# Kernel optimization log

Hardware: AMD Instinct MI355X
Metric: run time of the kernel (lower is better)

Reference implementation:

```python
import jax, jax.numpy as jnp
import numpy as np

R, A, K, N = 4096, 101, 32, 4000000
AEC_LOW, AEC_SPAN = 0.0, 1.0
ETA_NEON, ETA_CHILD, ETA_ADULT = 2.0, 1.5, 1.0
SINK_M = 0.5
FEMALE_SHARE = 0.5
THETA_DEV, PHI_REP, THETA_CYC = 1.0, 1.0, 5.0
RATE_ANN, KAPPA = 0.02, 1.0
WA, RA = 15, 65
INHERIT_CONC, INHERIT_FRAC, BIRTH_ENDOW = 1.0, 0.8, 1.0


def setup_inputs() -> dict:
    key = jax.random.key(0)
    ks = jax.random.split(key, 26)
    dt = 1.0 / 365.0
    pop_age = jax.random.uniform(ks[8], (R, A)) * 1e4
    aging_M = jnp.eye(A) * (1.0 - dt) + jnp.eye(A, A, k=1) * dt
    aging_M = aging_M.at[A - 1, A - 1].set(1.0)
    return {
        'aec_r': jax.random.uniform(ks[0], (R,)) * 2.0,
        'gdp_pc_r': jax.random.uniform(ks[1], (R,)) * 5e4 + 1e3,
        'gdp_pc_ema_R': jax.random.uniform(ks[2], (R,)) * 5e4 + 1e3,
        'gdp_pc_baseline_R': jax.random.uniform(ks[3], (R,)) * 5e4 + 1e3,
        'dev_index_R': jax.random.uniform(ks[4], (R,)),
        'sink_use': jax.random.uniform(ks[5], (R,)),
        'sink_cap': jax.random.uniform(ks[6], (R,)) + 0.5,
        'hazard_A_base': jax.random.uniform(ks[7], (A,)) * 0.1 + 0.001,
        'pop_age': pop_age,
        'population': pop_age.sum(axis=1),
        'aging_M': aging_M,
        'asfr_vector': jax.random.uniform(ks[9], (35,)) * 0.2,
        'distance': jax.random.uniform(ks[10], (R, R)) * 100.0 + 1.0,
        'consump_w_age': jax.random.uniform(ks[11], (A,)),
        'participation_w_age': jax.random.uniform(ks[12], (A,)),
        'consump_base_R': jax.random.uniform(ks[13], (R,)) * 1e4 + 1e3,
        'labor_base_R': jax.random.uniform(ks[14], (R,)) * 1e4 + 1e3,
        'greed': jax.random.uniform(ks[15], (N,)) + 0.01,
        'eATP': jax.random.uniform(ks[16], (N,)) * 100.0,
        'eADP': jax.random.uniform(ks[17], (N,)) * 100.0,
        'eAMP': jax.random.uniform(ks[18], (N,)) * 100.0,
        'pool_atp_R': jax.random.uniform(ks[19], (R,)) * 1e6,
        'pool_adp_R': jax.random.uniform(ks[20], (R,)) * 1e6,
        'pool_amp_R': jax.random.uniform(ks[21], (R,)) * 1e6,
        'nbr_idx': jax.random.randint(ks[22], (R, K), 0, R),
        'agent_region': jax.random.randint(ks[23], (N,), 0, R),
    }


def _forward(aec_r, gdp_pc_r, gdp_pc_ema_R, gdp_pc_baseline_R, dev_index_R, sink_use, sink_cap,
             hazard_A_base, pop_age, population, aging_M, asfr_vector, distance, consump_w_age,
             participation_w_age, consump_base_R, labor_base_R, greed, eATP, eADP, eAMP,
             pool_atp_R, pool_adp_R, pool_amp_R, nbr_idx, agent_region):
    eps = 1e-9
    dt = 1.0 / 365.0
    aec_norm = jnp.clip((aec_r - AEC_LOW) / AEC_SPAN, 0.0, 1.0)
    gdp_prev = gdp_pc_ema_R
    gdp_ema = gdp_prev * 0.9 + 0.1 * gdp_pc_r
    g_ratio = jnp.log(jnp.maximum(gdp_ema / (gdp_pc_baseline_R + eps), 1e-6))
    g_term = jnp.clip(0.5 + 0.5 * jnp.tanh(0.5 * g_ratio), 0.0, 1.0)
    util = jnp.clip(sink_use / (sink_cap + eps), 0.0, 1.0)
    H = jnp.clip(0.5 * aec_norm + 0.4 * g_term + 0.1 * (1.0 - util), 0.0, 1.0)
    dev_proxy = jnp.clip(0.5 + 0.5 * jnp.tanh(0.3 * g_ratio), 0.0, 1.0)
    dev = dev_index_R * 0.99 + 0.01 * dev_proxy
    # age-bucketed hazard multipliers: age 0 / ages 1..14 / ages 15+
    ages = jnp.arange(A)[None, :]
    m_neon = jnp.exp(-ETA_NEON * H)[:, None]
    m_child = jnp.exp(-ETA_CHILD * H)[:, None]
    m_adult = jnp.exp(-ETA_ADULT * H)[:, None]
    mult = jnp.where(ages == 0, m_neon, jnp.where(ages < 15, m_child, m_adult))
    haz = jnp.clip(hazard_A_base[None, :] * mult * (1.0 + SINK_M * util[:, None]), 0.0, 5.0)
    S = jnp.exp(-haz * dt)
    survivors = pop_age * S
    pop_after = survivors @ aging_M  # [R, A]
    deaths_R = jnp.maximum(pop_age.sum(1) - survivors.sum(1), 0.0)
    death_frac_R = jnp.clip(deaths_R / (population + eps), 0.0, 0.99)
    # fertility
    female_RF = FEMALE_SHARE * pop_after[:, 15:50]
    surv_u5 = jnp.exp(-haz[:, 0:5].sum(1))
    F_dev = jnp.clip(jnp.exp(-THETA_DEV * dev), 0.5, 1.5)
    F_rep = jnp.clip((0.995 / jnp.maximum(surv_u5, 1e-3)) ** PHI_REP, 0.5, 1.8)
    g_growth = jnp.log(jnp.maximum(gdp_ema + eps, 1e-6)) - jnp.log(jnp.maximum(gdp_prev + eps, 1e-6))
    F_cyc = jnp.clip(jnp.exp(-THETA_CYC * jnp.maximum(-g_growth, 0.0)), 0.6, 1.2)
    F_total = jnp.clip(F_dev * F_rep * F_cyc, 0.4, 1.8)
    births = jnp.maximum((female_RF * asfr_vector[None, :]).sum(1) * F_total * dt, 0.0)
    births_surv = births * jnp.exp(-haz[:, 0] * dt)
    pop_after = pop_after.at[:, 0].add(births_surv)
    # migration gather-scatter over neighbor regions
    a0, a1 = 18, 40
    mobile = pop_after[:, a0:a1]
    attract = 0.6 * (gdp_pc_r / (gdp_pc_baseline_R + eps)) + 0.4 * (0.5 + 0.5 * aec_norm)
    attract = attract / (attract.mean() + eps)
    dist = jnp.take_along_axis(distance, nbr_idx, axis=1)  # [R, K]
    cost = 1.0 + dist / (dist.mean() + eps)
    w = jax.nn.relu(attract[nbr_idx] / cost ** KAPPA)
    w = w / (w.sum(1, keepdims=True) + eps)
    frac_move = min(max(RATE_ANN * dt, 0.0), 0.25)
    out_R = mobile.sum(1) * frac_move
    move = out_R[:, None] * w  # [R, K]
    age_share = mobile / (mobile.sum(1, keepdims=True) + eps)
    pop_after = pop_after.at[:, a0:a1].add(-age_share * move.sum(1, keepdims=True))
    inflow = (age_share[:, None, :] * move[:, :, None]).reshape(R * K, a1 - a0)
    add = jnp.zeros((R, a1 - a0), pop_after.dtype).at[nbr_idx.reshape(-1)].add(inflow)
    pop_after = pop_after.at[:, a0:a1].add(add)
    pop_new = jnp.maximum(pop_after, 0.0)
    population_new = jnp.maximum(pop_new.sum(1), 0.0)
    consump_scale = jnp.clip((pop_new * consump_w_age[None, :]).sum(1) / (consump_base_R + eps), 0.25, 4.0)
    labor_factor = jnp.clip((pop_new * participation_w_age[None, :]).sum(1) / (labor_base_R + eps), 0.2, 1.2)
    work = pop_new[:, WA:RA].sum(1)
    young = pop_new[:, :WA].sum(1)
    old = pop_new[:, RA:].sum(1)
    psr = work / (old + eps)
    dep = (young + old) / (work + eps)
    # agent-level death / inheritance scatters
    dfi = death_frac_R[agent_region]
    w_raw = (greed + 1e-9) ** INHERIT_CONC
    w_sum_r = jax.ops.segment_sum(w_raw, agent_region, num_segments=R)
    w_norm = w_raw / (w_sum_r[agent_region] + eps)

    def settle(wallet, pool):
        removed = wallet * dfi
        removed_pool = jax.ops.segment_sum(removed, agent_region, num_segments=R)
        heir_pool = removed_pool * INHERIT_FRAC
        wallet2 = wallet - removed + w_norm * heir_pool[agent_region]
        return wallet2, pool - (removed_pool - heir_pool)

    eATP2, pool_atp2 = settle(eATP, pool_atp_R)
    eADP2, pool_adp2 = settle(eADP, pool_adp_R)
    eAMP2, pool_amp2 = settle(eAMP, pool_amp_R)
    counts = jax.ops.segment_sum(jnp.ones_like(dfi), agent_region, num_segments=R)
    eATP2 = eATP2 + BIRTH_ENDOW * (births_surv / jnp.maximum(counts, 1.0))[agent_region]
    return (pop_new, population_new, gdp_ema, dev, H, consump_scale, labor_factor, psr, dep,
            eATP2, eADP2, eAMP2, pool_atp2, pool_adp2, pool_amp2)


def reference(aec_r, gdp_pc_r, gdp_pc_ema_R, gdp_pc_baseline_R, dev_index_R, sink_use, sink_cap,
              hazard_A_base, pop_age, population, aging_M, asfr_vector, distance, consump_w_age,
              participation_w_age, consump_base_R, labor_base_R, greed, eATP, eADP, eAMP,
              pool_atp_R, pool_adp_R, pool_amp_R, nbr_idx, agent_region):
    return _forward(aec_r, gdp_pc_r, gdp_pc_ema_R, gdp_pc_baseline_R, dev_index_R, sink_use,
                    sink_cap, hazard_A_base, pop_age, population, aging_M, asfr_vector, distance,
                    consump_w_age, participation_w_age, consump_base_R, labor_base_R, greed,
                    eATP, eADP, eAMP, pool_atp_R, pool_adp_R, pool_amp_R, nbr_idx, agent_region)
```

## Files before the change

kernel.cpp:

```cpp
#include <hip/hip_runtime.h>

#define RR 4096
#define AA 101
#define PAD_W 104
#define KK 32
#define NAG 4000000

#define NCHUNK 32
#define DR 512
#define NRANGE 8
#define EPB (RR * KK / NCHUNK)
#define NB 512
#define NMIG (NRANGE * NCHUNK)
#define CH 16

static constexpr float EPS  = 1e-9f;
static constexpr float DT   = 1.0f / 365.0f;
static constexpr float FRAC_MOVE = 0.02f / 365.0f;

static constexpr float SC2   = 4.0f;
static constexpr float INV2  = 0.25f;
static constexpr float SC9   = 512.0f;
static constexpr float INV9  = 1.0f / 512.0f;
static constexpr float SC18  = 262144.0f;
static constexpr float INV18 = 1.0f / 262144.0f;

#define OUT_POP   0
#define OUT_POPN  413696
#define OUT_GDP   417792
#define OUT_DEV   421888
#define OUT_H     425984
#define OUT_CONS  430080
#define OUT_LAB   434176
#define OUT_PSR   438272
#define OUT_DEP   442368
#define OUT_ATP   446464
#define OUT_ADP   4446464
#define OUT_AMP   8446464
#define OUT_PATP  12446464
#define OUT_PADP  12450560
#define OUT_PAMP  12454656

static __device__ __forceinline__ float clampf(float x, float lo, float hi) {
    return fminf(fmaxf(x, lo), hi);
}
static __device__ __forceinline__ float wred(float x) {
#pragma unroll
    for (int m = 32; m; m >>= 1) x += __shfl_xor(x, m);
    return x;
}

__global__ __launch_bounds__(256) void k_region1(
    const float* __restrict__ aec, const float* __restrict__ gdp_pc,
    const float* __restrict__ gdp_ema_in, const float* __restrict__ gdp_base,
    const float* __restrict__ dev_in, const float* __restrict__ sink_use,
    const float* __restrict__ sink_cap, const float* __restrict__ haz_base,
    const float* __restrict__ pop_age, const float* __restrict__ population,
    const float* __restrict__ aging, const float* __restrict__ asfr,
    const float* __restrict__ distance, const int* __restrict__ nbr,
    float* __restrict__ Wpa, float* __restrict__ Wdfrac, float* __restrict__ Wbsurv,
    float* __restrict__ Wattr, float* __restrict__ Wgdist, float* __restrict__ Wdsum,
    float* __restrict__ O)
{
    int wid = threadIdx.x >> 6, lane = threadIdx.x & 63;
    int r = blockIdx.x * 4 + wid;

    float aec_norm = clampf(aec[r], 0.0f, 1.0f);
    float gprev = gdp_ema_in[r];
    float gema  = gprev * 0.9f + 0.1f * gdp_pc[r];
    float base  = gdp_base[r];
    float g_ratio = logf(fmaxf(gema / (base + EPS), 1e-6f));
    float g_term  = clampf(0.5f + 0.5f * tanhf(0.5f * g_ratio), 0.0f, 1.0f);
    float util = clampf(sink_use[r] / (sink_cap[r] + EPS), 0.0f, 1.0f);
    float H = clampf(0.5f * aec_norm + 0.4f * g_term + 0.1f * (1.0f - util), 0.0f, 1.0f);
    float dev_proxy = clampf(0.5f + 0.5f * tanhf(0.3f * g_ratio), 0.0f, 1.0f);
    float dev = dev_in[r] * 0.99f + 0.01f * dev_proxy;

    float m_neon  = expf(-2.0f * H);
    float m_child = expf(-1.5f * H);
    float m_adult = expf(-1.0f * H);
    float hazmul = 1.0f + 0.5f * util;

    int a0 = lane * 2, a1 = a0 + 1;
    bool v0 = (a0 < AA), v1 = (a1 < AA);

    float p0 = 0.f, p1 = 0.f, hz0 = 0.f, hz1 = 0.f;
    if (v0) {
        p0 = pop_age[r * AA + a0];
        float mult = (a0 == 0) ? m_neon : ((a0 < 15) ? m_child : m_adult);
        hz0 = clampf(haz_base[a0] * mult * hazmul, 0.0f, 5.0f);
    }
    if (v1) {
        p1 = pop_age[r * AA + a1];
        float mult = (a1 < 15) ? m_child : m_adult;
        hz1 = clampf(haz_base[a1] * mult * hazmul, 0.0f, 5.0f);
    }
    float s0 = v0 ? p0 * expf(-hz0 * DT) : 0.f;
    float s1 = v1 ? p1 * expf(-hz1 * DT) : 0.f;
    float sp = __shfl_up(s1, 1);

    float Md0 = 0.f, Md1 = 0.f, Ms0 = 0.f, Ms1 = 0.f;
    if (v0) { Md0 = aging[a0 * AA + a0]; if (a0 > 0) Ms0 = aging[(a0 - 1) * AA + a0]; }
    if (v1) { Md1 = aging[a1 * AA + a1]; Ms1 = aging[(a1 - 1) * AA + a1]; }

    float pa0 = v0 ? ((a0 == 0) ? s0 * Md0 : s0 * Md0 + sp * Ms0) : 0.f;
    float pa1 = v1 ? (s1 * Md1 + s0 * Ms1) : 0.f;

    if (v0 && a0 > 0) Wpa[r * PAD_W + a0] = pa0;
    if (v1)           Wpa[r * PAD_W + a1] = pa1;

    float pop_sum  = wred(p0 + p1);
    float surv_sum = wred(s0 + s1);
    float haz05 = wred(((v0 && a0 < 5) ? hz0 : 0.f) + ((v1 && a1 < 5) ? hz1 : 0.f));
    float bs0 = (a0 >= 15 && a0 < 50) ? 0.5f * pa0 * asfr[a0 - 15] : 0.f;
    float bs1 = (a1 >= 15 && a1 < 50) ? 0.5f * pa1 * asfr[a1 - 15] : 0.f;
    float b_sum = wred(bs0 + bs1);

    float dc = 0.f;
    if (lane < KK) {
        int idx = nbr[r * KK + lane];
        float d = distance[(size_t)r * RR + idx];
        Wgdist[r * KK + lane] = d;
        dc = d;
    }
    float dsum = wred(dc);

    if (lane == 0) {
        O[OUT_GDP + r] = gema;
        O[OUT_DEV + r] = dev;
        O[OUT_H + r]   = H;

        float deaths = fmaxf(pop_sum - surv_sum, 0.0f);
        Wdfrac[r] = clampf(deaths / (population[r] + EPS), 0.0f, 0.99f);

        float surv_u5 = expf(-haz05);
        float F_dev = clampf(expf(-dev), 0.5f, 1.5f);
        float F_rep = clampf(0.995f / fmaxf(surv_u5, 0.001f), 0.5f, 1.8f);
        float g_growth = logf(fmaxf(gema + EPS, 1e-6f)) - logf(fmaxf(gprev + EPS, 1e-6f));
        float F_cyc = clampf(expf(-5.0f * fmaxf(-g_growth, 0.0f)), 0.6f, 1.2f);
        float F_total = clampf(F_dev * F_rep * F_cyc, 0.4f, 1.8f);
        float births = fmaxf(b_sum * F_total * DT, 0.0f);
        float bsurv = births * expf(-hz0 * DT);
        Wbsurv[r] = bsurv;
        Wpa[r * PAD_W + 0] = pa0 + bsurv;

        Wattr[r] = 0.6f * (gdp_pc[r] / (base + EPS)) + 0.4f * (0.5f + 0.5f * aec_norm);
        Wdsum[r] = dsum;
    }
}

__global__ __launch_bounds__(256) void k_migrate_a(
    const int* __restrict__ nbr, const float* __restrict__ Wattr,
    const float* __restrict__ Wgdist, const float* __restrict__ Wdsum,
    float* __restrict__ Wpa, float* __restrict__ Wash, float* __restrict__ Wmove)
{
    __shared__ float sred[8];
    int t = threadIdx.x;
    {
        float a = 0.f, d = 0.f;
        for (int i = t; i < RR; i += 256) { a += Wattr[i]; d += Wdsum[i]; }
        a = wred(a); d = wred(d);
        int w0 = t >> 6;
        if ((t & 63) == 0) { sred[w0] = a; sred[4 + w0] = d; }
    }
    __syncthreads();
    float asum = sred[0] + sred[1] + sred[2] + sred[3];
    float dall = sred[4] + sred[5] + sred[6] + sred[7];
    float inv_am = 1.0f / (asum / (float)RR + EPS);
    float inv_dm = 1.0f / (dall / (float)(RR * KK) + EPS);

    int wid = t >> 6, lane = t & 63;
    int r = blockIdx.x * 4 + wid;

    float mob = 0.f;
    if (lane < 22) mob = Wpa[r * PAD_W + 18 + lane];
    float msum = wred(lane < 22 ? mob : 0.f);

    float w = 0.f;
    if (lane < KK) {
        int idx = nbr[r * KK + lane];
        float an = Wattr[idx] * inv_am;
        float cost = 1.0f + Wgdist[r * KK + lane] * inv_dm;
        w = fmaxf(an / cost, 0.0f);
    }
    float wsum = wred(lane < KK ? w : 0.f);

    float out_R = msum * FRAC_MOVE;
    float invw = 1.0f / (wsum + EPS);
    float move_sum = out_R * wsum * invw;
    float inv_ms = 1.0f / (msum + EPS);

    if (lane < 22) {
        float ash = mob * inv_ms;
        Wash[r * 22 + lane] = ash;
        Wpa[r * PAD_W + 18 + lane] = mob - ash * move_sum;
    }
    if (lane < KK) Wmove[r * KK + lane] = out_R * w * invw;
}

__global__ __launch_bounds__(512) void k_migbhist(
    const int* __restrict__ nbr, const float* __restrict__ Wash,
    const float* __restrict__ Wmove, float* __restrict__ Smig,
    const int* __restrict__ reg, const float* __restrict__ greed,
    const float* __restrict__ atp, const float* __restrict__ adp,
    const float* __restrict__ amp, unsigned long long* __restrict__ S)
{
    __shared__ unsigned long long h[11 * DR];
    int bid = blockIdx.x;

    if (bid < NMIG) {
        int range = bid & (NRANGE - 1);
        int chunk = bid >> 3;
        int d0 = range * DR;

        for (int i = threadIdx.x; i < 11 * DR; i += 512) h[i] = 0ull;
        __syncthreads();

        int tend = (chunk + 1) * EPB;
        for (int t = chunk * EPB + threadIdx.x; t < tend; t += 512) {
            int idx = nbr[t];
            if (idx >= d0 && idx < d0 + DR) {
                int rsrc = t >> 5;
                float mv = Wmove[t];
                const float* ash = &Wash[rsrc * 22];
                int dl = idx - d0;
#pragma unroll
                for (int f = 0; f < 11; f++) {
                    unsigned long long lo = __float2uint_rn(ash[2 * f] * mv * SC18);
                    unsigned long long hi = __float2uint_rn(ash[2 * f + 1] * mv * SC18);
                    atomicAdd(&h[f * DR + dl], lo | (hi << 32));
                }
            }
        }
        __syncthreads();

        for (int i = threadIdx.x; i < 11 * DR; i += 512) {
            int f = i / DR, d = i - f * DR;
            unsigned long long v = h[i];
            Smig[(chunk * 22 + 2 * f) * RR + d0 + d]     = (float)(unsigned int)v * INV18;
            Smig[(chunk * 22 + 2 * f + 1) * RR + d0 + d] = (float)(v >> 32) * INV18;
        }
    } else {
        int b = bid - NMIG;
        for (int i = threadIdx.x; i < RR; i += 512) h[i] = 0ull;
        __syncthreads();

        const int4*   reg4 = (const int4*)reg;
        const float4* g4 = (const float4*)greed;
        const float4* a4 = (const float4*)atp;
        const float4* d4 = (const float4*)adp;
        const float4* m4 = (const float4*)amp;
        const int NQ = NAG / 4;
        const int STRIDE = NB * 512;

        for (int q = b * 512 + threadIdx.x; q < NQ; q += STRIDE) {
            int4 rr = reg4[q];
            float4 gv = g4[q], av = a4[q], dv = d4[q], mv = m4[q];
#define DO1(RX, GX, AX, DX, MX) { \
            unsigned long long ai = __float2uint_rn((AX) * SC2); \
            unsigned long long di = __float2uint_rn((DX) * SC2); \
            unsigned long long mi = __float2uint_rn((MX) * SC2); \
            unsigned long long gi = __float2uint_rn(((GX) + 1e-9f) * SC9); \
            atomicAdd(&h[RX], ai | (di << 14) | (mi << 28) | (gi << 42) | (1ull << 56)); }
            DO1(rr.x, gv.x, av.x, dv.x, mv.x)
            DO1(rr.y, gv.y, av.y, dv.y, mv.y)
            DO1(rr.z, gv.z, av.z, dv.z, mv.z)
            DO1(rr.w, gv.w, av.w, dv.w, mv.w)
#undef DO1
        }
        __syncthreads();

        for (int i = threadIdx.x; i < RR; i += 512)
            S[(size_t)b * RR + i] = h[i];
    }
}

__global__ __launch_bounds__(256) void k_reduce(
    const unsigned long long* __restrict__ S, const float* __restrict__ Smig,
    float* __restrict__ T, float* __restrict__ Wadd)
{
    int blk = blockIdx.x;
    if (blk < 256) {
        int tid = blk * 256 + threadIdx.x;
        int r = tid & (RR - 1);
        int c = tid >> 12;
        const int bpc = NB / CH;
        float sa = 0.f, sd = 0.f, sm = 0.f, sg = 0.f, sc = 0.f;
        for (int b = c * bpc; b < (c + 1) * bpc; b++) {
            unsigned long long p = S[(size_t)b * RR + r];
            sa += (float)(unsigned int)(p & 0x3FFFull);
            sd += (float)(unsigned int)((p >> 14) & 0x3FFFull);
            sm += (float)(unsigned int)((p >> 28) & 0x3FFFull);
            sg += (float)(unsigned int)((p >> 42) & 0x3FFFull);
            sc += (float)(unsigned int)(p >> 56);
        }
        T[(0 * CH + c) * RR + r] = sa * INV2;
        T[(1 * CH + c) * RR + r] = sd * INV2;
        T[(2 * CH + c) * RR + r] = sm * INV2;
        T[(3 * CH + c) * RR + r] = sg * INV9;
        T[(4 * CH + c) * RR + r] = sc;
    } else {
        int t2 = (blk - 256) * 256 + threadIdx.x;
        int f = t2 >> 12, rr = t2 & (RR - 1);
        float acc = 0.f;
#pragma unroll
        for (int c = 0; c < NCHUNK; c++)
            acc += Smig[(c * 22 + f) * RR + rr];
        Wadd[rr * 24 + f] = acc;
    }
}

__global__ __launch_bounds__(256) void k_fin(
    const float* __restrict__ Wpa, const float* __restrict__ Wadd,
    const float* __restrict__ cw, const float* __restrict__ pw,
    const float* __restrict__ cbase, const float* __restrict__ lbase,
    const float* __restrict__ T,
    const float* __restrict__ Wdfrac, const float* __restrict__ Wbsurv,
    const float* __restrict__ patp, const float* __restrict__ padp,
    const float* __restrict__ pamp,
    float4* __restrict__ P4, float2* __restrict__ P2,
    float* __restrict__ O)
{
    int blk = blockIdx.x;
    if (blk < 1024) {
        int wid = threadIdx.x >> 6, lane = threadIdx.x & 63;
        int r = blk * 4 + wid;
        int a0 = lane * 2, a1 = a0 + 1;
        bool v0 = (a0 < AA), v1 = (a1 < AA);

        float va = 0.f, vb = 0.f;
        if (lane < 51) {
            float2 pp = *(const float2*)&Wpa[r * PAD_W + a0];
            va = pp.x; vb = pp.y;
        }
        if (a0 >= 18 && a0 < 40) {
            float2 ad = *(const float2*)&Wadd[r * 24 + (a0 - 18)];
            va += ad.x; vb += ad.y;
        }
        va = v0 ? fmaxf(va, 0.0f) : 0.f;
        vb = v1 ? fmaxf(vb, 0.0f) : 0.f;
        if (v0) O[OUT_POP + r * AA + a0] = va;
        if (v1) O[OUT_POP + r * AA + a1] = vb;

        float cw0 = v0 ? cw[a0] : 0.f, cw1 = v1 ? cw[a1] : 0.f;
        float pw0 = v0 ? pw[a0] : 0.f, pw1 = v1 ? pw[a1] : 0.f;

        float psum  = wred(va + vb);
        float cdot  = wred(va * cw0 + vb * cw1);
        float ldot  = wred(va * pw0 + vb * pw1);
        float young = wred(((a0 < 15) ? va : 0.f) + ((a1 < 15) ? vb : 0.f));
        float work  = wred(((a0 >= 15 && a0 < 65) ? va : 0.f) + ((a1 >= 15 && a1 < 65) ? vb : 0.f));
        float old   = wred(((a0 >= 65) ? va : 0.f) + ((a1 >= 65) ? vb : 0.f));

        if (lane == 0) {
            O[OUT_POPN + r] = fmaxf(psum, 0.0f);
            O[OUT_CONS + r] = clampf(cdot / (cbase[r] + EPS), 0.25f, 4.0f);
            O[OUT_LAB + r]  = clampf(ldot / (lbase[r] + EPS), 0.2f, 1.2f);
            O[OUT_PSR + r]  = work / (old + EPS);
            O[OUT_DEP + r]  = (young + old) / (work + EPS);
        }
    } else {
        int r = (blk - 1024) * 256 + threadIdx.x;
        if (r >= RR) return;
        float sums[5];
#pragma unroll
        for (int s = 0; s < 5; s++) {
            float acc = 0.f;
#pragma unroll
            for (int c = 0; c < CH; c++)
                acc += T[(s * CH + c) * RR + r];
            sums[s] = acc;
        }
        float dfi = Wdfrac[r];
        float ra = sums[0] * dfi;
        float rd = sums[1] * dfi;
        float rm = sums[2] * dfi;
        O[OUT_PATP + r] = patp[r] - ra * 0.2f;
        O[OUT_PADP + r] = padp[r] - rd * 0.2f;
        O[OUT_PAMP + r] = pamp[r] - rm * 0.2f;
        P4[r] = make_float4(1.0f - dfi, 1.0f / (sums[3] + EPS), ra * 0.8f, rd * 0.8f);
        P2[r] = make_float2(rm * 0.8f, Wbsurv[r] / fmaxf(sums[4], 1.0f));
    }
}

__global__ __launch_bounds__(256) void k_apply(
    const int* __restrict__ reg, const float* __restrict__ greed,
    const float* __restrict__ atp, const float* __restrict__ adp,
    const float* __restrict__ amp,
    const float4* __restrict__ P4, const float2* __restrict__ P2,
    float* __restrict__ O)
{
    int q = blockIdx.x * 256 + threadIdx.x;
    if (q >= NAG / 4) return;
    int4 rr = ((const int4*)reg)[q];
    float4 g = ((const float4*)greed)[q];
    float4 a = ((const float4*)atp)[q];
    float4 d = ((const float4*)adp)[q];
    float4 m = ((const float4*)amp)[q];
    float4 oa, od, om;
#define ONE(c) { float4 t4 = P4[rr.c]; float2 t2 = P2[rr.c]; \
    float wn = (g.c + 1e-9f) * t4.y; \
    oa.c = a.c * t4.x + wn * t4.z + t2.y; \
    od.c = d.c * t4.x + wn * t4.w; \
    om.c = m.c * t4.x + wn * t2.x; }
    ONE(x) ONE(y) ONE(z) ONE(w)
#undef ONE
    ((float4*)(O + OUT_ATP))[q] = oa;
    ((float4*)(O + OUT_ADP))[q] = od;
    ((float4*)(O + OUT_AMP))[q] = om;
}

extern "C" void kernel_launch(void* const* d_in, const int* in_sizes, int n_in,
                              void* d_out, int out_size, void* d_ws, size_t ws_size,
                              hipStream_t stream) {
    const float* aec       = (const float*)d_in[0];
    const float* gdp_pc    = (const float*)d_in[1];
    const float* gdp_ema   = (const float*)d_in[2];
    const float* gdp_base  = (const float*)d_in[3];
    const float* dev_in    = (const float*)d_in[4];
    const float* sink_use  = (const float*)d_in[5];
    const float* sink_cap  = (const float*)d_in[6];
    const float* haz_base  = (const float*)d_in[7];
    const float* pop_age   = (const float*)d_in[8];
    const float* population= (const float*)d_in[9];
    const float* aging     = (const float*)d_in[10];
    const float* asfr      = (const float*)d_in[11];
    const float* distance  = (const float*)d_in[12];
    const float* cw        = (const float*)d_in[13];
    const float* pw        = (const float*)d_in[14];
    const float* cbase     = (const float*)d_in[15];
    const float* lbase     = (const float*)d_in[16];
    const float* greed     = (const float*)d_in[17];
    const float* eATP      = (const float*)d_in[18];
    const float* eADP      = (const float*)d_in[19];
    const float* eAMP      = (const float*)d_in[20];
    const float* patp      = (const float*)d_in[21];
    const float* padp      = (const float*)d_in[22];
    const float* pamp      = (const float*)d_in[23];
    const int*   nbr       = (const int*)d_in[24];
    const int*   reg       = (const int*)d_in[25];

    float* O = (float*)d_out;

    float* W = (float*)d_ws;
    float* Wpa    = W;
    float* Wdfrac = Wpa    + RR * PAD_W;
    float* Wbsurv = Wdfrac + RR;
    float* Wattr  = Wbsurv + RR;
    float* Wdsum  = Wattr  + RR;
    float* Wgdist = Wdsum  + RR;
    float* Wash   = Wgdist + RR * KK;
    float* Wmove  = Wash   + RR * 22;
    float* P4f    = Wmove  + RR * KK;
    float* P2f    = P4f    + RR * 4;
    float* Wadd   = P2f    + RR * 2;
    float* T      = Wadd   + RR * 24;
    float* Smig   = T      + 5 * CH * RR;
    unsigned long long* S = (unsigned long long*)(Smig + (size_t)NCHUNK * 22 * RR);

    k_region1<<<RR / 4, 256, 0, stream>>>(
        aec, gdp_pc, gdp_ema, gdp_base, dev_in, sink_use, sink_cap, haz_base,
        pop_age, population, aging, asfr, distance, nbr,
        Wpa, Wdfrac, Wbsurv, Wattr, Wgdist, Wdsum, O);

    k_migrate_a<<<RR / 4, 256, 0, stream>>>(nbr, Wattr, Wgdist, Wdsum, Wpa, Wash, Wmove);

    k_migbhist<<<NMIG + NB, 512, 0, stream>>>(
        nbr, Wash, Wmove, Smig, reg, greed, eATP, eADP, eAMP, S);

    k_reduce<<<256 + (22 * RR) / 256, 256, 0, stream>>>(S, Smig, T, Wadd);

    k_fin<<<1024 + RR / 256, 256, 0, stream>>>(
        Wpa, Wadd, cw, pw, cbase, lbase, T, Wdfrac, Wbsurv,
        patp, padp, pamp, (float4*)P4f, (float2*)P2f, O);

    k_apply<<<(NAG / 4 + 255) / 256, 256, 0, stream>>>(
        reg, greed, eATP, eADP, eAMP, (const float4*)P4f, (const float2*)P2f, O);
}
```

Measured before the change: 97.12 us.

## Move agent histogram into region kernel and regroup reduce stages

The per-agent packed-atomic histogram moves out of the migration kernel and into the first region kernel as extra blocks. It now runs alongside the per-region demography and no longer waits for the migration-weight stage. The histogram loop now prefetches the next strided iteration's loads before doing the current iteration's atomics. The S-to-T reduction moves into the migration-scatter kernel's trailing blocks, and the Smig fold becomes its own kernel, so the launch count stays the same. The first kernel's shared memory grows to 32KB for all blocks, which may lower occupancy for the region blocks.

```diff
diff --git a/kernel.cpp b/kernel.cpp
--- a/kernel.cpp
+++ b/kernel.cpp
@@ -50,7 +50,7 @@
     return x;
 }
 
-__global__ __launch_bounds__(256) void k_region1(
+__global__ __launch_bounds__(256) void k_r1hist(
     const float* __restrict__ aec, const float* __restrict__ gdp_pc,
     const float* __restrict__ gdp_ema_in, const float* __restrict__ gdp_base,
     const float* __restrict__ dev_in, const float* __restrict__ sink_use,
@@ -60,92 +60,143 @@
     const float* __restrict__ distance, const int* __restrict__ nbr,
     float* __restrict__ Wpa, float* __restrict__ Wdfrac, float* __restrict__ Wbsurv,
     float* __restrict__ Wattr, float* __restrict__ Wgdist, float* __restrict__ Wdsum,
+    const int* __restrict__ reg, const float* __restrict__ greed,
+    const float* __restrict__ atp, const float* __restrict__ adp,
+    const float* __restrict__ amp, unsigned long long* __restrict__ S,
     float* __restrict__ O)
 {
-    int wid = threadIdx.x >> 6, lane = threadIdx.x & 63;
-    int r = blockIdx.x * 4 + wid;
-
-    float aec_norm = clampf(aec[r], 0.0f, 1.0f);
-    float gprev = gdp_ema_in[r];
-    float gema  = gprev * 0.9f + 0.1f * gdp_pc[r];
-    float base  = gdp_base[r];
-    float g_ratio = logf(fmaxf(gema / (base + EPS), 1e-6f));
-    float g_term  = clampf(0.5f + 0.5f * tanhf(0.5f * g_ratio), 0.0f, 1.0f);
-    float util = clampf(sink_use[r] / (sink_cap[r] + EPS), 0.0f, 1.0f);
-    float H = clampf(0.5f * aec_norm + 0.4f * g_term + 0.1f * (1.0f - util), 0.0f, 1.0f);
-    float dev_proxy = clampf(0.5f + 0.5f * tanhf(0.3f * g_ratio), 0.0f, 1.0f);
-    float dev = dev_in[r] * 0.99f + 0.01f * dev_proxy;
-
-    float m_neon  = expf(-2.0f * H);
-    float m_child = expf(-1.5f * H);
-    float m_adult = expf(-1.0f * H);
-    float hazmul = 1.0f + 0.5f * util;
-
-    int a0 = lane * 2, a1 = a0 + 1;
-    bool v0 = (a0 < AA), v1 = (a1 < AA);
-
-    float p0 = 0.f, p1 = 0.f, hz0 = 0.f, hz1 = 0.f;
-    if (v0) {
-        p0 = pop_age[r * AA + a0];
-        float mult = (a0 == 0) ? m_neon : ((a0 < 15) ? m_child : m_adult);
-        hz0 = clampf(haz_base[a0] * mult * hazmul, 0.0f, 5.0f);
-    }
-    if (v1) {
-        p1 = pop_age[r * AA + a1];
-        float mult = (a1 < 15) ? m_child : m_adult;
-        hz1 = clampf(haz_base[a1] * mult * hazmul, 0.0f, 5.0f);
-    }
-    float s0 = v0 ? p0 * expf(-hz0 * DT) : 0.f;
-    float s1 = v1 ? p1 * expf(-hz1 * DT) : 0.f;
-    float sp = __shfl_up(s1, 1);
-
-    float Md0 = 0.f, Md1 = 0.f, Ms0 = 0.f, Ms1 = 0.f;
-    if (v0) { Md0 = aging[a0 * AA + a0]; if (a0 > 0) Ms0 = aging[(a0 - 1) * AA + a0]; }
-    if (v1) { Md1 = aging[a1 * AA + a1]; Ms1 = aging[(a1 - 1) * AA + a1]; }
-
-    float pa0 = v0 ? ((a0 == 0) ? s0 * Md0 : s0 * Md0 + sp * Ms0) : 0.f;
-    float pa1 = v1 ? (s1 * Md1 + s0 * Ms1) : 0.f;
-
-    if (v0 && a0 > 0) Wpa[r * PAD_W + a0] = pa0;
-    if (v1)           Wpa[r * PAD_W + a1] = pa1;
-
-    float pop_sum  = wred(p0 + p1);
-    float surv_sum = wred(s0 + s1);
-    float haz05 = wred(((v0 && a0 < 5) ? hz0 : 0.f) + ((v1 && a1 < 5) ? hz1 : 0.f));
-    float bs0 = (a0 >= 15 && a0 < 50) ? 0.5f * pa0 * asfr[a0 - 15] : 0.f;
-    float bs1 = (a1 >= 15 && a1 < 50) ? 0.5f * pa1 * asfr[a1 - 15] : 0.f;
-    float b_sum = wred(bs0 + bs1);
-
-    float dc = 0.f;
-    if (lane < KK) {
-        int idx = nbr[r * KK + lane];
-        float d = distance[(size_t)r * RR + idx];
-        Wgdist[r * KK + lane] = d;
-        dc = d;
-    }
-    float dsum = wred(dc);
-
-    if (lane == 0) {
-        O[OUT_GDP + r] = gema;
-        O[OUT_DEV + r] = dev;
-        O[OUT_H + r]   = H;
-
-        float deaths = fmaxf(pop_sum - surv_sum, 0.0f);
-        Wdfrac[r] = clampf(deaths / (population[r] + EPS), 0.0f, 0.99f);
-
-        float surv_u5 = expf(-haz05);
-        float F_dev = clampf(expf(-dev), 0.5f, 1.5f);
-        float F_rep = clampf(0.995f / fmaxf(surv_u5, 0.001f), 0.5f, 1.8f);
-        float g_growth = logf(fmaxf(gema + EPS, 1e-6f)) - logf(fmaxf(gprev + EPS, 1e-6f));
-        float F_cyc = clampf(expf(-5.0f * fmaxf(-g_growth, 0.0f)), 0.6f, 1.2f);
-        float F_total = clampf(F_dev * F_rep * F_cyc, 0.4f, 1.8f);
-        float births = fmaxf(b_sum * F_total * DT, 0.0f);
-        float bsurv = births * expf(-hz0 * DT);
-        Wbsurv[r] = bsurv;
-        Wpa[r * PAD_W + 0] = pa0 + bsurv;
-
-        Wattr[r] = 0.6f * (gdp_pc[r] / (base + EPS)) + 0.4f * (0.5f + 0.5f * aec_norm);
-        Wdsum[r] = dsum;
+    __shared__ unsigned long long h[RR];
+    int blk = blockIdx.x;
+
+    if (blk < 1024) {
+        int wid = threadIdx.x >> 6, lane = threadIdx.x & 63;
+        int r = blk * 4 + wid;
+
+        float aec_norm = clampf(aec[r], 0.0f, 1.0f);
+        float gprev = gdp_ema_in[r];
+        float gema  = gprev * 0.9f + 0.1f * gdp_pc[r];
+        float base  = gdp_base[r];
+        float g_ratio = logf(fmaxf(gema / (base + EPS), 1e-6f));
+        float g_term  = clampf(0.5f + 0.5f * tanhf(0.5f * g_ratio), 0.0f, 1.0f);
+        float util = clampf(sink_use[r] / (sink_cap[r] + EPS), 0.0f, 1.0f);
+        float H = clampf(0.5f * aec_norm + 0.4f * g_term + 0.1f * (1.0f - util), 0.0f, 1.0f);
+        float dev_proxy = clampf(0.5f + 0.5f * tanhf(0.3f * g_ratio), 0.0f, 1.0f);
+        float dev = dev_in[r] * 0.99f + 0.01f * dev_proxy;
+
+        float m_neon  = expf(-2.0f * H);
+        float m_child = expf(-1.5f * H);
+        float m_adult = expf(-1.0f * H);
+        float hazmul = 1.0f + 0.5f * util;
+
+        int a0 = lane * 2, a1 = a0 + 1;
+        bool v0 = (a0 < AA), v1 = (a1 < AA);
+
+        float p0 = 0.f, p1 = 0.f, hz0 = 0.f, hz1 = 0.f;
+        if (v0) {
+            p0 = pop_age[r * AA + a0];
+            float mult = (a0 == 0) ? m_neon : ((a0 < 15) ? m_child : m_adult);
+            hz0 = clampf(haz_base[a0] * mult * hazmul, 0.0f, 5.0f);
+        }
+        if (v1) {
+            p1 = pop_age[r * AA + a1];
+            float mult = (a1 < 15) ? m_child : m_adult;
+            hz1 = clampf(haz_base[a1] * mult * hazmul, 0.0f, 5.0f);
+        }
+        float s0 = v0 ? p0 * expf(-hz0 * DT) : 0.f;
+        float s1 = v1 ? p1 * expf(-hz1 * DT) : 0.f;
+        float sp = __shfl_up(s1, 1);
+
+        float Md0 = 0.f, Md1 = 0.f, Ms0 = 0.f, Ms1 = 0.f;
+        if (v0) { Md0 = aging[a0 * AA + a0]; if (a0 > 0) Ms0 = aging[(a0 - 1) * AA + a0]; }
+        if (v1) { Md1 = aging[a1 * AA + a1]; Ms1 = aging[(a1 - 1) * AA + a1]; }
+
+        float pa0 = v0 ? ((a0 == 0) ? s0 * Md0 : s0 * Md0 + sp * Ms0) : 0.f;
+        float pa1 = v1 ? (s1 * Md1 + s0 * Ms1) : 0.f;
+
+        if (v0 && a0 > 0) Wpa[r * PAD_W + a0] = pa0;
+        if (v1)           Wpa[r * PAD_W + a1] = pa1;
+
+        float pop_sum  = wred(p0 + p1);
+        float surv_sum = wred(s0 + s1);
+        float haz05 = wred(((v0 && a0 < 5) ? hz0 : 0.f) + ((v1 && a1 < 5) ? hz1 : 0.f));
+        float bs0 = (a0 >= 15 && a0 < 50) ? 0.5f * pa0 * asfr[a0 - 15] : 0.f;
+        float bs1 = (a1 >= 15 && a1 < 50) ? 0.5f * pa1 * asfr[a1 - 15] : 0.f;
+        float b_sum = wred(bs0 + bs1);
+
+        float dc = 0.f;
+        if (lane < KK) {
+            int idx = nbr[r * KK + lane];
+            float d = distance[(size_t)r * RR + idx];
+            Wgdist[r * KK + lane] = d;
+            dc = d;
+        }
+        float dsum = wred(dc);
+
+        if (lane == 0) {
+            O[OUT_GDP + r] = gema;
+            O[OUT_DEV + r] = dev;
+            O[OUT_H + r]   = H;
+
+            float deaths = fmaxf(pop_sum - surv_sum, 0.0f);
+            Wdfrac[r] = clampf(deaths / (population[r] + EPS), 0.0f, 0.99f);
+
+            float surv_u5 = expf(-haz05);
+            float F_dev = clampf(expf(-dev), 0.5f, 1.5f);
+            float F_rep = clampf(0.995f / fmaxf(surv_u5, 0.001f), 0.5f, 1.8f);
+            float g_growth = logf(fmaxf(gema + EPS, 1e-6f)) - logf(fmaxf(gprev + EPS, 1e-6f));
+            float F_cyc = clampf(expf(-5.0f * fmaxf(-g_growth, 0.0f)), 0.6f, 1.2f);
+            float F_total = clampf(F_dev * F_rep * F_cyc, 0.4f, 1.8f);
+            float births = fmaxf(b_sum * F_total * DT, 0.0f);
+            float bsurv = births * expf(-hz0 * DT);
+            Wbsurv[r] = bsurv;
+            Wpa[r * PAD_W + 0] = pa0 + bsurv;
+
+            Wattr[r] = 0.6f * (gdp_pc[r] / (base + EPS)) + 0.4f * (0.5f + 0.5f * aec_norm);
+            Wdsum[r] = dsum;
+        }
+    } else {
+        int b = blk - 1024;
+        for (int i = threadIdx.x; i < RR; i += 256) h[i] = 0ull;
+        __syncthreads();
+
+        const int4*   reg4 = (const int4*)reg;
+        const float4* g4 = (const float4*)greed;
+        const float4* a4 = (const float4*)atp;
+        const float4* d4 = (const float4*)adp;
+        const float4* m4 = (const float4*)amp;
+        const int NQ = NAG / 4;
+        const int STRIDE = NB * 256;
+
+        int q = b * 256 + threadIdx.x;
+        if (q < NQ) {
+            int4 rA = reg4[q];
+            float4 gA = g4[q], aA = a4[q], dA = d4[q], mA = m4[q];
+            while (true) {
+                int qn = q + STRIDE;
+                bool more = (qn < NQ);
+                int qs = more ? qn : q;
+                int4 rB = reg4[qs];
+                float4 gB = g4[qs], aB = a4[qs], dB = d4[qs], mB = m4[qs];
+#define DO1(RX, GX, AX, DX, MX) { \
+                unsigned long long ai = __float2uint_rn((AX) * SC2); \
+                unsigned long long di = __float2uint_rn((DX) * SC2); \
+                unsigned long long mi = __float2uint_rn((MX) * SC2); \
+                unsigned long long gi = __float2uint_rn(((GX) + 1e-9f) * SC9); \
+                atomicAdd(&h[RX], ai | (di << 14) | (mi << 28) | (gi << 42) | (1ull << 56)); }
+                DO1(rA.x, gA.x, aA.x, dA.x, mA.x)
+                DO1(rA.y, gA.y, aA.y, dA.y, mA.y)
+                DO1(rA.z, gA.z, aA.z, dA.z, mA.z)
+                DO1(rA.w, gA.w, aA.w, dA.w, mA.w)
+#undef DO1
+                if (!more) break;
+                rA = rB; gA = gB; aA = aB; dA = dB; mA = mB;
+                q = qn;
+            }
+        }
+        __syncthreads();
+
+        for (int i = threadIdx.x; i < RR; i += 256)
+            S[(size_t)b * RR + i] = h[i];
     }
 }
 
@@ -198,12 +249,10 @@
     if (lane < KK) Wmove[r * KK + lane] = out_R * w * invw;
 }
 
-__global__ __launch_bounds__(512) void k_migbhist(
+__global__ __launch_bounds__(512) void k_mbdec(
     const int* __restrict__ nbr, const float* __restrict__ Wash,
     const float* __restrict__ Wmove, float* __restrict__ Smig,
-    const int* __restrict__ reg, const float* __restrict__ greed,
-    const float* __restrict__ atp, const float* __restrict__ adp,
-    const float* __restrict__ amp, unsigned long long* __restrict__ S)
+    const unsigned long long* __restrict__ S, float* __restrict__ T)
 {
     __shared__ unsigned long long h[11 * DR];
     int bid = blockIdx.x;
@@ -241,47 +290,7 @@
             Smig[(chunk * 22 + 2 * f + 1) * RR + d0 + d] = (float)(v >> 32) * INV18;
         }
     } else {
-        int b = bid - NMIG;
-        for (int i = threadIdx.x; i < RR; i += 512) h[i] = 0ull;
-        __syncthreads();
-
-        const int4*   reg4 = (const int4*)reg;
-        const float4* g4 = (const float4*)greed;
-        const float4* a4 = (const float4*)atp;
-        const float4* d4 = (const float4*)adp;
-        const float4* m4 = (const float4*)amp;
-        const int NQ = NAG / 4;
-        const int STRIDE = NB * 512;
-
-        for (int q = b * 512 + threadIdx.x; q < NQ; q += STRIDE) {
-            int4 rr = reg4[q];
-            float4 gv = g4[q], av = a4[q], dv = d4[q], mv = m4[q];
-#define DO1(RX, GX, AX, DX, MX) { \
-            unsigned long long ai = __float2uint_rn((AX) * SC2); \
-            unsigned long long di = __float2uint_rn((DX) * SC2); \
-            unsigned long long mi = __float2uint_rn((MX) * SC2); \
-            unsigned long long gi = __float2uint_rn(((GX) + 1e-9f) * SC9); \
-            atomicAdd(&h[RX], ai | (di << 14) | (mi << 28) | (gi << 42) | (1ull << 56)); }
-            DO1(rr.x, gv.x, av.x, dv.x, mv.x)
-            DO1(rr.y, gv.y, av.y, dv.y, mv.y)
-            DO1(rr.z, gv.z, av.z, dv.z, mv.z)
-            DO1(rr.w, gv.w, av.w, dv.w, mv.w)
-#undef DO1
-        }
-        __syncthreads();
-
-        for (int i = threadIdx.x; i < RR; i += 512)
-            S[(size_t)b * RR + i] = h[i];
-    }
-}
-
-__global__ __launch_bounds__(256) void k_reduce(
-    const unsigned long long* __restrict__ S, const float* __restrict__ Smig,
-    float* __restrict__ T, float* __restrict__ Wadd)
-{
-    int blk = blockIdx.x;
-    if (blk < 256) {
-        int tid = blk * 256 + threadIdx.x;
+        int tid = (bid - NMIG) * 512 + threadIdx.x;
         int r = tid & (RR - 1);
         int c = tid >> 12;
         const int bpc = NB / CH;
@@ -299,15 +308,19 @@
         T[(2 * CH + c) * RR + r] = sm * INV2;
         T[(3 * CH + c) * RR + r] = sg * INV9;
         T[(4 * CH + c) * RR + r] = sc;
-    } else {
-        int t2 = (blk - 256) * 256 + threadIdx.x;
-        int f = t2 >> 12, rr = t2 & (RR - 1);
-        float acc = 0.f;
+    }
+}
+
+__global__ __launch_bounds__(256) void k_fold(
+    const float* __restrict__ Smig, float* __restrict__ Wadd)
+{
+    int t2 = blockIdx.x * 256 + threadIdx.x;
+    int f = t2 >> 12, rr = t2 & (RR - 1);
+    float acc = 0.f;
 #pragma unroll
-        for (int c = 0; c < NCHUNK; c++)
-            acc += Smig[(c * 22 + f) * RR + rr];
-        Wadd[rr * 24 + f] = acc;
-    }
+    for (int c = 0; c < NCHUNK; c++)
+        acc += Smig[(c * 22 + f) * RR + rr];
+    Wadd[rr * 24 + f] = acc;
 }
 
 __global__ __launch_bounds__(256) void k_fin(
@@ -458,17 +471,17 @@
     float* Smig   = T      + 5 * CH * RR;
     unsigned long long* S = (unsigned long long*)(Smig + (size_t)NCHUNK * 22 * RR);
 
-    k_region1<<<RR / 4, 256, 0, stream>>>(
+    k_r1hist<<<1024 + NB, 256, 0, stream>>>(
         aec, gdp_pc, gdp_ema, gdp_base, dev_in, sink_use, sink_cap, haz_base,
         pop_age, population, aging, asfr, distance, nbr,
-        Wpa, Wdfrac, Wbsurv, Wattr, Wgdist, Wdsum, O);
+        Wpa, Wdfrac, Wbsurv, Wattr, Wgdist, Wdsum,
+        reg, greed, eATP, eADP, eAMP, S, O);
 
     k_migrate_a<<<RR / 4, 256, 0, stream>>>(nbr, Wattr, Wgdist, Wdsum, Wpa, Wash, Wmove);
 
-    k_migbhist<<<NMIG + NB, 512, 0, stream>>>(
-        nbr, Wash, Wmove, Smig, reg, greed, eATP, eADP, eAMP, S);
-
-    k_reduce<<<256 + (22 * RR) / 256, 256, 0, stream>>>(S, Smig, T, Wadd);
+    k_mbdec<<<NMIG + 128, 512, 0, stream>>>(nbr, Wash, Wmove, Smig, S, T);
+
+    k_fold<<<(22 * RR) / 256, 256, 0, stream>>>(Smig, Wadd);
 
     k_fin<<<1024 + RR / 256, 256, 0, stream>>>(
         Wpa, Wadd, cw, pw, cbase, lbase, T, Wdfrac, Wbsurv,
```

New measurement: 92.81 us. 1.05x faster.

## Move agent histogram into region kernel and decode S alongside migration

Applied to the files above, without the earlier changes.

The per-agent packed shared-memory histogram moves out of the migration kernel into the first region kernel. Both now run as 1024-thread blocks in one launch, so the 4M-agent streaming pass overlaps with the per-region demographics instead of running after migrate_a. The S decode (per-chunk summation into T) moves into the migration kernel's extra blocks, and the Smig fold becomes its own small kernel. The launch count stays the same, but block sizes and the dependency order change, and the 1024-thread blocks may lower occupancy.

```diff
diff --git a/kernel.cpp b/kernel.cpp
--- a/kernel.cpp
+++ b/kernel.cpp
@@ -50,7 +50,7 @@
     return x;
 }
 
-__global__ __launch_bounds__(256) void k_region1(
+__global__ __launch_bounds__(1024) void k_r1hist(
     const float* __restrict__ aec, const float* __restrict__ gdp_pc,
     const float* __restrict__ gdp_ema_in, const float* __restrict__ gdp_base,
     const float* __restrict__ dev_in, const float* __restrict__ sink_use,
@@ -60,92 +60,132 @@
     const float* __restrict__ distance, const int* __restrict__ nbr,
     float* __restrict__ Wpa, float* __restrict__ Wdfrac, float* __restrict__ Wbsurv,
     float* __restrict__ Wattr, float* __restrict__ Wgdist, float* __restrict__ Wdsum,
+    const int* __restrict__ reg, const float* __restrict__ greed,
+    const float* __restrict__ atp, const float* __restrict__ adp,
+    const float* __restrict__ amp, unsigned long long* __restrict__ S,
     float* __restrict__ O)
 {
-    int wid = threadIdx.x >> 6, lane = threadIdx.x & 63;
-    int r = blockIdx.x * 4 + wid;
-
-    float aec_norm = clampf(aec[r], 0.0f, 1.0f);
-    float gprev = gdp_ema_in[r];
-    float gema  = gprev * 0.9f + 0.1f * gdp_pc[r];
-    float base  = gdp_base[r];
-    float g_ratio = logf(fmaxf(gema / (base + EPS), 1e-6f));
-    float g_term  = clampf(0.5f + 0.5f * tanhf(0.5f * g_ratio), 0.0f, 1.0f);
-    float util = clampf(sink_use[r] / (sink_cap[r] + EPS), 0.0f, 1.0f);
-    float H = clampf(0.5f * aec_norm + 0.4f * g_term + 0.1f * (1.0f - util), 0.0f, 1.0f);
-    float dev_proxy = clampf(0.5f + 0.5f * tanhf(0.3f * g_ratio), 0.0f, 1.0f);
-    float dev = dev_in[r] * 0.99f + 0.01f * dev_proxy;
-
-    float m_neon  = expf(-2.0f * H);
-    float m_child = expf(-1.5f * H);
-    float m_adult = expf(-1.0f * H);
-    float hazmul = 1.0f + 0.5f * util;
-
-    int a0 = lane * 2, a1 = a0 + 1;
-    bool v0 = (a0 < AA), v1 = (a1 < AA);
-
-    float p0 = 0.f, p1 = 0.f, hz0 = 0.f, hz1 = 0.f;
-    if (v0) {
-        p0 = pop_age[r * AA + a0];
-        float mult = (a0 == 0) ? m_neon : ((a0 < 15) ? m_child : m_adult);
-        hz0 = clampf(haz_base[a0] * mult * hazmul, 0.0f, 5.0f);
-    }
-    if (v1) {
-        p1 = pop_age[r * AA + a1];
-        float mult = (a1 < 15) ? m_child : m_adult;
-        hz1 = clampf(haz_base[a1] * mult * hazmul, 0.0f, 5.0f);
-    }
-    float s0 = v0 ? p0 * expf(-hz0 * DT) : 0.f;
-    float s1 = v1 ? p1 * expf(-hz1 * DT) : 0.f;
-    float sp = __shfl_up(s1, 1);
-
-    float Md0 = 0.f, Md1 = 0.f, Ms0 = 0.f, Ms1 = 0.f;
-    if (v0) { Md0 = aging[a0 * AA + a0]; if (a0 > 0) Ms0 = aging[(a0 - 1) * AA + a0]; }
-    if (v1) { Md1 = aging[a1 * AA + a1]; Ms1 = aging[(a1 - 1) * AA + a1]; }
-
-    float pa0 = v0 ? ((a0 == 0) ? s0 * Md0 : s0 * Md0 + sp * Ms0) : 0.f;
-    float pa1 = v1 ? (s1 * Md1 + s0 * Ms1) : 0.f;
-
-    if (v0 && a0 > 0) Wpa[r * PAD_W + a0] = pa0;
-    if (v1)           Wpa[r * PAD_W + a1] = pa1;
-
-    float pop_sum  = wred(p0 + p1);
-    float surv_sum = wred(s0 + s1);
-    float haz05 = wred(((v0 && a0 < 5) ? hz0 : 0.f) + ((v1 && a1 < 5) ? hz1 : 0.f));
-    float bs0 = (a0 >= 15 && a0 < 50) ? 0.5f * pa0 * asfr[a0 - 15] : 0.f;
-    float bs1 = (a1 >= 15 && a1 < 50) ? 0.5f * pa1 * asfr[a1 - 15] : 0.f;
-    float b_sum = wred(bs0 + bs1);
-
-    float dc = 0.f;
-    if (lane < KK) {
-        int idx = nbr[r * KK + lane];
-        float d = distance[(size_t)r * RR + idx];
-        Wgdist[r * KK + lane] = d;
-        dc = d;
-    }
-    float dsum = wred(dc);
-
-    if (lane == 0) {
-        O[OUT_GDP + r] = gema;
-        O[OUT_DEV + r] = dev;
-        O[OUT_H + r]   = H;
-
-        float deaths = fmaxf(pop_sum - surv_sum, 0.0f);
-        Wdfrac[r] = clampf(deaths / (population[r] + EPS), 0.0f, 0.99f);
-
-        float surv_u5 = expf(-haz05);
-        float F_dev = clampf(expf(-dev), 0.5f, 1.5f);
-        float F_rep = clampf(0.995f / fmaxf(surv_u5, 0.001f), 0.5f, 1.8f);
-        float g_growth = logf(fmaxf(gema + EPS, 1e-6f)) - logf(fmaxf(gprev + EPS, 1e-6f));
-        float F_cyc = clampf(expf(-5.0f * fmaxf(-g_growth, 0.0f)), 0.6f, 1.2f);
-        float F_total = clampf(F_dev * F_rep * F_cyc, 0.4f, 1.8f);
-        float births = fmaxf(b_sum * F_total * DT, 0.0f);
-        float bsurv = births * expf(-hz0 * DT);
-        Wbsurv[r] = bsurv;
-        Wpa[r * PAD_W + 0] = pa0 + bsurv;
-
-        Wattr[r] = 0.6f * (gdp_pc[r] / (base + EPS)) + 0.4f * (0.5f + 0.5f * aec_norm);
-        Wdsum[r] = dsum;
+    __shared__ unsigned long long h[RR];
+    int blk = blockIdx.x;
+
+    if (blk < 256) {
+        int wid = threadIdx.x >> 6, lane = threadIdx.x & 63;
+        int r = blk * 16 + wid;
+
+        float aec_norm = clampf(aec[r], 0.0f, 1.0f);
+        float gprev = gdp_ema_in[r];
+        float gema  = gprev * 0.9f + 0.1f * gdp_pc[r];
+        float base  = gdp_base[r];
+        float g_ratio = logf(fmaxf(gema / (base + EPS), 1e-6f));
+        float g_term  = clampf(0.5f + 0.5f * tanhf(0.5f * g_ratio), 0.0f, 1.0f);
+        float util = clampf(sink_use[r] / (sink_cap[r] + EPS), 0.0f, 1.0f);
+        float H = clampf(0.5f * aec_norm + 0.4f * g_term + 0.1f * (1.0f - util), 0.0f, 1.0f);
+        float dev_proxy = clampf(0.5f + 0.5f * tanhf(0.3f * g_ratio), 0.0f, 1.0f);
+        float dev = dev_in[r] * 0.99f + 0.01f * dev_proxy;
+
+        float m_neon  = expf(-2.0f * H);
+        float m_child = expf(-1.5f * H);
+        float m_adult = expf(-1.0f * H);
+        float hazmul = 1.0f + 0.5f * util;
+
+        int a0 = lane * 2, a1 = a0 + 1;
+        bool v0 = (a0 < AA), v1 = (a1 < AA);
+
+        float p0 = 0.f, p1 = 0.f, hz0 = 0.f, hz1 = 0.f;
+        if (v0) {
+            p0 = pop_age[r * AA + a0];
+            float mult = (a0 == 0) ? m_neon : ((a0 < 15) ? m_child : m_adult);
+            hz0 = clampf(haz_base[a0] * mult * hazmul, 0.0f, 5.0f);
+        }
+        if (v1) {
+            p1 = pop_age[r * AA + a1];
+            float mult = (a1 < 15) ? m_child : m_adult;
+            hz1 = clampf(haz_base[a1] * mult * hazmul, 0.0f, 5.0f);
+        }
+        float s0 = v0 ? p0 * expf(-hz0 * DT) : 0.f;
+        float s1 = v1 ? p1 * expf(-hz1 * DT) : 0.f;
+        float sp = __shfl_up(s1, 1);
+
+        float Md0 = 0.f, Md1 = 0.f, Ms0 = 0.f, Ms1 = 0.f;
+        if (v0) { Md0 = aging[a0 * AA + a0]; if (a0 > 0) Ms0 = aging[(a0 - 1) * AA + a0]; }
+        if (v1) { Md1 = aging[a1 * AA + a1]; Ms1 = aging[(a1 - 1) * AA + a1]; }
+
+        float pa0 = v0 ? ((a0 == 0) ? s0 * Md0 : s0 * Md0 + sp * Ms0) : 0.f;
+        float pa1 = v1 ? (s1 * Md1 + s0 * Ms1) : 0.f;
+
+        if (v0 && a0 > 0) Wpa[r * PAD_W + a0] = pa0;
+        if (v1)           Wpa[r * PAD_W + a1] = pa1;
+
+        float pop_sum  = wred(p0 + p1);
+        float surv_sum = wred(s0 + s1);
+        float haz05 = wred(((v0 && a0 < 5) ? hz0 : 0.f) + ((v1 && a1 < 5) ? hz1 : 0.f));
+        float bs0 = (a0 >= 15 && a0 < 50) ? 0.5f * pa0 * asfr[a0 - 15] : 0.f;
+        float bs1 = (a1 >= 15 && a1 < 50) ? 0.5f * pa1 * asfr[a1 - 15] : 0.f;
+        float b_sum = wred(bs0 + bs1);
+
+        float dc = 0.f;
+        if (lane < KK) {
+            int idx = nbr[r * KK + lane];
+            float d = distance[(size_t)r * RR + idx];
+            Wgdist[r * KK + lane] = d;
+            dc = d;
+        }
+        float dsum = wred(dc);
+
+        if (lane == 0) {
+            O[OUT_GDP + r] = gema;
+            O[OUT_DEV + r] = dev;
+            O[OUT_H + r]   = H;
+
+            float deaths = fmaxf(pop_sum - surv_sum, 0.0f);
+            Wdfrac[r] = clampf(deaths / (population[r] + EPS), 0.0f, 0.99f);
+
+            float surv_u5 = expf(-haz05);
+            float F_dev = clampf(expf(-dev), 0.5f, 1.5f);
+            float F_rep = clampf(0.995f / fmaxf(surv_u5, 0.001f), 0.5f, 1.8f);
+            float g_growth = logf(fmaxf(gema + EPS, 1e-6f)) - logf(fmaxf(gprev + EPS, 1e-6f));
+            float F_cyc = clampf(expf(-5.0f * fmaxf(-g_growth, 0.0f)), 0.6f, 1.2f);
+            float F_total = clampf(F_dev * F_rep * F_cyc, 0.4f, 1.8f);
+            float births = fmaxf(b_sum * F_total * DT, 0.0f);
+            float bsurv = births * expf(-hz0 * DT);
+            Wbsurv[r] = bsurv;
+            Wpa[r * PAD_W + 0] = pa0 + bsurv;
+
+            Wattr[r] = 0.6f * (gdp_pc[r] / (base + EPS)) + 0.4f * (0.5f + 0.5f * aec_norm);
+            Wdsum[r] = dsum;
+        }
+    } else {
+        int b = blk - 256;
+        for (int i = threadIdx.x; i < RR; i += 1024) h[i] = 0ull;
+        __syncthreads();
+
+        const int4*   reg4 = (const int4*)reg;
+        const float4* g4 = (const float4*)greed;
+        const float4* a4 = (const float4*)atp;
+        const float4* d4 = (const float4*)adp;
+        const float4* m4 = (const float4*)amp;
+        const int NQ = NAG / 4;
+        const int STRIDE = NB * 1024;
+
+        for (int q = b * 1024 + threadIdx.x; q < NQ; q += STRIDE) {
+            int4 rr = reg4[q];
+            float4 gv = g4[q], av = a4[q], dv = d4[q], mv = m4[q];
+#define DO1(RX, GX, AX, DX, MX) { \
+            unsigned long long ai = __float2uint_rn((AX) * SC2); \
+            unsigned long long di = __float2uint_rn((DX) * SC2); \
+            unsigned long long mi = __float2uint_rn((MX) * SC2); \
+            unsigned long long gi = __float2uint_rn(((GX) + 1e-9f) * SC9); \
+            atomicAdd(&h[RX], ai | (di << 14) | (mi << 28) | (gi << 42) | (1ull << 56)); }
+            DO1(rr.x, gv.x, av.x, dv.x, mv.x)
+            DO1(rr.y, gv.y, av.y, dv.y, mv.y)
+            DO1(rr.z, gv.z, av.z, dv.z, mv.z)
+            DO1(rr.w, gv.w, av.w, dv.w, mv.w)
+#undef DO1
+        }
+        __syncthreads();
+
+        for (int i = threadIdx.x; i < RR; i += 1024)
+            S[(size_t)b * RR + i] = h[i];
     }
 }
 
@@ -198,12 +238,10 @@
     if (lane < KK) Wmove[r * KK + lane] = out_R * w * invw;
 }
 
-__global__ __launch_bounds__(512) void k_migbhist(
+__global__ __launch_bounds__(512) void k_mbdec(
     const int* __restrict__ nbr, const float* __restrict__ Wash,
     const float* __restrict__ Wmove, float* __restrict__ Smig,
-    const int* __restrict__ reg, const float* __restrict__ greed,
-    const float* __restrict__ atp, const float* __restrict__ adp,
-    const float* __restrict__ amp, unsigned long long* __restrict__ S)
+    const unsigned long long* __restrict__ S, float* __restrict__ T)
 {
     __shared__ unsigned long long h[11 * DR];
     int bid = blockIdx.x;
@@ -241,47 +279,7 @@
             Smig[(chunk * 22 + 2 * f + 1) * RR + d0 + d] = (float)(v >> 32) * INV18;
         }
     } else {
-        int b = bid - NMIG;
-        for (int i = threadIdx.x; i < RR; i += 512) h[i] = 0ull;
-        __syncthreads();
-
-        const int4*   reg4 = (const int4*)reg;
-        const float4* g4 = (const float4*)greed;
-        const float4* a4 = (const float4*)atp;
-        const float4* d4 = (const float4*)adp;
-        const float4* m4 = (const float4*)amp;
-        const int NQ = NAG / 4;
-        const int STRIDE = NB * 512;
-
-        for (int q = b * 512 + threadIdx.x; q < NQ; q += STRIDE) {
-            int4 rr = reg4[q];
-            float4 gv = g4[q], av = a4[q], dv = d4[q], mv = m4[q];
-#define DO1(RX, GX, AX, DX, MX) { \
-            unsigned long long ai = __float2uint_rn((AX) * SC2); \
-            unsigned long long di = __float2uint_rn((DX) * SC2); \
-            unsigned long long mi = __float2uint_rn((MX) * SC2); \
-            unsigned long long gi = __float2uint_rn(((GX) + 1e-9f) * SC9); \
-            atomicAdd(&h[RX], ai | (di << 14) | (mi << 28) | (gi << 42) | (1ull << 56)); }
-            DO1(rr.x, gv.x, av.x, dv.x, mv.x)
-            DO1(rr.y, gv.y, av.y, dv.y, mv.y)
-            DO1(rr.z, gv.z, av.z, dv.z, mv.z)
-            DO1(rr.w, gv.w, av.w, dv.w, mv.w)
-#undef DO1
-        }
-        __syncthreads();
-
-        for (int i = threadIdx.x; i < RR; i += 512)
-            S[(size_t)b * RR + i] = h[i];
-    }
-}
-
-__global__ __launch_bounds__(256) void k_reduce(
-    const unsigned long long* __restrict__ S, const float* __restrict__ Smig,
-    float* __restrict__ T, float* __restrict__ Wadd)
-{
-    int blk = blockIdx.x;
-    if (blk < 256) {
-        int tid = blk * 256 + threadIdx.x;
+        int tid = (bid - NMIG) * 512 + threadIdx.x;
         int r = tid & (RR - 1);
         int c = tid >> 12;
         const int bpc = NB / CH;
@@ -299,15 +297,19 @@
         T[(2 * CH + c) * RR + r] = sm * INV2;
         T[(3 * CH + c) * RR + r] = sg * INV9;
         T[(4 * CH + c) * RR + r] = sc;
-    } else {
-        int t2 = (blk - 256) * 256 + threadIdx.x;
-        int f = t2 >> 12, rr = t2 & (RR - 1);
-        float acc = 0.f;
+    }
+}
+
+__global__ __launch_bounds__(256) void k_fold(
+    const float* __restrict__ Smig, float* __restrict__ Wadd)
+{
+    int t2 = blockIdx.x * 256 + threadIdx.x;
+    int f = t2 >> 12, rr = t2 & (RR - 1);
+    float acc = 0.f;
 #pragma unroll
-        for (int c = 0; c < NCHUNK; c++)
-            acc += Smig[(c * 22 + f) * RR + rr];
-        Wadd[rr * 24 + f] = acc;
-    }
+    for (int c = 0; c < NCHUNK; c++)
+        acc += Smig[(c * 22 + f) * RR + rr];
+    Wadd[rr * 24 + f] = acc;
 }
 
 __global__ __launch_bounds__(256) void k_fin(
@@ -458,17 +460,17 @@
     float* Smig   = T      + 5 * CH * RR;
     unsigned long long* S = (unsigned long long*)(Smig + (size_t)NCHUNK * 22 * RR);
 
-    k_region1<<<RR / 4, 256, 0, stream>>>(
+    k_r1hist<<<256 + NB, 1024, 0, stream>>>(
         aec, gdp_pc, gdp_ema, gdp_base, dev_in, sink_use, sink_cap, haz_base,
         pop_age, population, aging, asfr, distance, nbr,
-        Wpa, Wdfrac, Wbsurv, Wattr, Wgdist, Wdsum, O);
+        Wpa, Wdfrac, Wbsurv, Wattr, Wgdist, Wdsum,
+        reg, greed, eATP, eADP, eAMP, S, O);
 
     k_migrate_a<<<RR / 4, 256, 0, stream>>>(nbr, Wattr, Wgdist, Wdsum, Wpa, Wash, Wmove);
 
-    k_migbhist<<<NMIG + NB, 512, 0, stream>>>(
-        nbr, Wash, Wmove, Smig, reg, greed, eATP, eADP, eAMP, S);
-
-    k_reduce<<<256 + (22 * RR) / 256, 256, 0, stream>>>(S, Smig, T, Wadd);
+    k_mbdec<<<NMIG + 128, 512, 0, stream>>>(nbr, Wash, Wmove, Smig, S, T);
+
+    k_fold<<<(22 * RR) / 256, 256, 0, stream>>>(Smig, Wadd);
 
     k_fin<<<1024 + RR / 256, 256, 0, stream>>>(
         Wpa, Wadd, cw, pw, cbase, lbase, T, Wdfrac, Wbsurv,
```

New measurement: 89.59 us. -7.8%, faster.
